# Kernel optimization log

Measured on AMD Instinct MI355X. Metric: run time of the kernel, lower is better.

## Reference

```python
import jax, jax.numpy as jnp
import numpy as np
import math

D_MODEL = 1024
N_HEADS = 16
D_K = D_MODEL // N_HEADS
BS, SQ, SK = 2, 2048, 2048


def setup_inputs() -> dict:
    key = jax.random.key(0)
    ks = jax.random.split(key, 7)
    q = jax.random.normal(ks[0], (BS, SQ, D_MODEL), dtype=jnp.float32)
    k = jax.random.normal(ks[1], (BS, SK, D_MODEL), dtype=jnp.float32)
    v = jax.random.normal(ks[2], (BS, SK, D_MODEL), dtype=jnp.float32)
    # causal mask: True = masked out (matches torch masked_fill semantics)
    mask = jnp.broadcast_to(
        ~jnp.tril(jnp.ones((SQ, SK), dtype=bool)), (BS, SQ, SK))
    scale = 1.0 / math.sqrt(D_MODEL)
    wq = jax.random.normal(ks[3], (D_MODEL, D_MODEL), dtype=jnp.float32) * scale
    wk = jax.random.normal(ks[4], (D_MODEL, D_MODEL), dtype=jnp.float32) * scale
    wv = jax.random.normal(ks[5], (D_MODEL, D_MODEL), dtype=jnp.float32) * scale
    wo = jax.random.normal(ks[6], (D_MODEL, D_MODEL), dtype=jnp.float32) * scale
    return {"q": q, "k": k, "v": v, "mask": mask,
            "wq": wq, "wk": wk, "wv": wv, "wo": wo}


def reference(q, k, v, mask, wq, wk, wv, wo):
    bs, sq, _ = q.shape
    sk = k.shape[1]
    # nn.Linear(bias=False): x @ W.T ; reshape to heads -> [b, h, s, d_k]
    qh = (q @ wq.T).reshape(bs, sq, N_HEADS, D_K).transpose(0, 2, 1, 3)
    kh = (k @ wk.T).reshape(bs, sk, N_HEADS, D_K).transpose(0, 2, 1, 3)
    vh = (v @ wv.T).reshape(bs, sk, N_HEADS, D_K).transpose(0, 2, 1, 3)
    # scaled dot-product attention, full [b,h,sq,sk] scores (as original)
    z = jnp.einsum('bhqd,bhkd->bhqk', qh, kh) / math.sqrt(D_K)
    z = jnp.where(mask[:, None, :, :], jnp.float32(-1e10), z)
    z = jax.nn.softmax(z, axis=-1)
    z = jnp.einsum('bhqk,bhkd->bhqd', z, vh)
    z = z.transpose(0, 2, 1, 3).reshape(bs, sq, D_MODEL)
    return z @ wo.T
```

## Files before the change

kernel.cpp:

```cpp
#include <hip/hip_runtime.h>
#include <hip/hip_bf16.h>
#include <stdint.h>

typedef short s16x8 __attribute__((ext_vector_type(8)));
typedef float f32x4 __attribute__((ext_vector_type(4)));

#define BSZ 2
#define SQL 2048
#define DMODEL 1024
#define NHEAD 16
#define DKH 64

#if __has_builtin(__builtin_amdgcn_exp2f)
#define EXP2(x) __builtin_amdgcn_exp2f(x)
#else
#define EXP2(x) exp2f(x)
#endif

__device__ __forceinline__ ushort f2bf(float f) {
  uint32_t u = __float_as_uint(f);
  u += 0x7fffu + ((u >> 16) & 1u);
  return (ushort)(u >> 16);
}

__device__ __forceinline__ uint32_t cvtpk_bf16(float lo, float hi) {
  uint32_t r;
  asm("v_cvt_pk_bf16_f32 %0, %1, %2" : "=v"(r) : "v"(lo), "v"(hi));
  return r;
}

__device__ __forceinline__ float rowmax16(float x) {
  x = fmaxf(x, __int_as_float(__builtin_amdgcn_update_dpp(0, __float_as_int(x), 0x121, 0xf, 0xf, true)));
  x = fmaxf(x, __int_as_float(__builtin_amdgcn_update_dpp(0, __float_as_int(x), 0x122, 0xf, 0xf, true)));
  x = fmaxf(x, __int_as_float(__builtin_amdgcn_update_dpp(0, __float_as_int(x), 0x124, 0xf, 0xf, true)));
  x = fmaxf(x, __int_as_float(__builtin_amdgcn_update_dpp(0, __float_as_int(x), 0x128, 0xf, 0xf, true)));
  return x;
}

__device__ __forceinline__ void gload_lds16(const ushort* g, ushort* l) {
  __builtin_amdgcn_global_load_lds((const __attribute__((address_space(1))) void*)g,
                                   (__attribute__((address_space(3))) void*)l,
                                   16, 0, 0);
}

__global__ void cvt_w(const float* __restrict__ wq, const float* __restrict__ wk,
                      const float* __restrict__ wv, const float* __restrict__ wo,
                      ushort* __restrict__ dwq, ushort* __restrict__ dwk,
                      ushort* __restrict__ dwv, ushort* __restrict__ dwo) {
  const float* s = (blockIdx.y == 0) ? wq : (blockIdx.y == 1) ? wk : (blockIdx.y == 2) ? wv : wo;
  ushort* d = (blockIdx.y == 0) ? dwq : (blockIdx.y == 1) ? dwk : (blockIdx.y == 2) ? dwv : dwo;
  int i = (blockIdx.x * 256 + threadIdx.x) * 4;
  float4 x = *(const float4*)(s + i);
  ushort4 o;
  o.x = f2bf(x.x); o.y = f2bf(x.y); o.z = f2bf(x.z); o.w = f2bf(x.w);
  *(ushort4*)(d + i) = o;
}

__device__ __forceinline__ void epi_heads(f32x4 (&acc)[4][4], ushort* D, float scale, bool vtrans) {
  const int lane = threadIdx.x & 63, w = threadIdx.x >> 6;
  const int m0 = blockIdx.x * 128, n0 = blockIdx.y * 128;
  const int wm = (w >> 1) * 64, wn = (w & 1) * 64;
#pragma unroll
  for (int mi = 0; mi < 4; ++mi)
#pragma unroll
    for (int ni = 0; ni < 4; ++ni)
#pragma unroll
      for (int r = 0; r < 4; ++r) {
        int m = m0 + wm + mi * 16 + (lane >> 4) * 4 + r;
        int n = n0 + wn + ni * 16 + (lane & 15);
        ushort bv = f2bf(acc[mi][ni][r] * scale);
        int b = m >> 11, s = m & 2047, h = n >> 6, d = n & 63;
        if (vtrans) {
          int sp = (s & ~63) | (((s & 15) << 2) | ((s >> 4) & 3));
          D[((size_t)((b * 16 + h) * 64 + d)) * 2048 + sp] = bv;
        } else {
          D[((size_t)((b * 16 + h) * 2048 + s)) * 64 + d] = bv;
        }
      }
}

__global__ __launch_bounds__(256) void gemm_qkv(const float* __restrict__ qf,
                                                const float* __restrict__ kf,
                                                const float* __restrict__ vf,
                                                const ushort* __restrict__ wqb,
                                                const ushort* __restrict__ wkb,
                                                const ushort* __restrict__ wvb,
                                                ushort* __restrict__ Qh,
                                                ushort* __restrict__ Kh,
                                                ushort* __restrict__ Vt) {
  __shared__ __align__(16) float sA32[2 * 4096];
  __shared__ __align__(16) ushort sB[2 * 4096];
  const int z = blockIdx.z;
  const float* A = (z == 0) ? qf : (z == 1) ? kf : vf;
  const ushort* B = (z == 0) ? wqb : (z == 1) ? wkb : wvb;
  const int t = threadIdx.x, w = t >> 6, lane = t & 63;
  const int lrow = lane & 15, g = lane >> 4;
  const int swzB = (lrow >> 1) & 3;
  const int m0 = blockIdx.x * 128, n0 = blockIdx.y * 128;
  const int wm = (w >> 1) * 64, wn = (w & 1) * 64;
  f32x4 acc[4][4] = {};

  auto stage = [&](int kt, int buf) {
#pragma unroll
    for (int i2 = 0; i2 < 4; ++i2) {
      int ci = i2 * 256 + t;
      int row = ci >> 3;
      int fc = (ci & 7) ^ (row & 7);
      gload_lds16((const ushort*)(A + (size_t)(m0 + row) * 1024 + kt * 32 + fc * 4),
                  (ushort*)(sA32 + buf * 4096 + (i2 * 256 + w * 64) * 4));
    }
#pragma unroll
    for (int i2 = 0; i2 < 2; ++i2) {
      int ci = i2 * 256 + t;
      int row = ci >> 2;
      int cs = (ci & 3) ^ ((row >> 1) & 3);
      gload_lds16(B + (size_t)(n0 + row) * 1024 + kt * 32 + cs * 8,
                  sB + buf * 4096 + (i2 * 256 + w * 64) * 8);
    }
  };

  stage(0, 0);
  for (int kt = 0; kt < 32; ++kt) {
    const int cur = kt & 1;
    if (kt < 31) {
      stage(kt + 1, cur ^ 1);
      asm volatile("s_waitcnt vmcnt(6)" ::: "memory");
    } else {
      asm volatile("s_waitcnt vmcnt(0)" ::: "memory");
    }
    __builtin_amdgcn_s_barrier();
    __builtin_amdgcn_sched_barrier(0);
    const float* pA = sA32 + cur * 4096;
    const ushort* pB = sB + cur * 4096;
    const int gs = (g ^ swzB) * 8;
    s16x8 af[4], bfr[4];
#pragma unroll
    for (int mi = 0; mi < 4; ++mi) {
      int row = wm + mi * 16 + lrow;
      int f0 = (2 * g) ^ (row & 7);
      int f1 = (2 * g + 1) ^ (row & 7);
      f32x4 x0 = *(const f32x4*)(pA + row * 32 + f0 * 4);
      f32x4 x1 = *(const f32x4*)(pA + row * 32 + f1 * 4);
      union { uint32_t u[4]; s16x8 v; } cc;
      cc.u[0] = cvtpk_bf16(x0[0], x0[1]);
      cc.u[1] = cvtpk_bf16(x0[2], x0[3]);
      cc.u[2] = cvtpk_bf16(x1[0], x1[1]);
      cc.u[3] = cvtpk_bf16(x1[2], x1[3]);
      af[mi] = cc.v;
    }
#pragma unroll
    for (int ni = 0; ni < 4; ++ni)
      bfr[ni] = *(const s16x8*)(pB + (wn + ni * 16 + lrow) * 32 + gs);
    __builtin_amdgcn_s_setprio(1);
#pragma unroll
    for (int mi = 0; mi < 4; ++mi)
#pragma unroll
      for (int ni = 0; ni < 4; ++ni)
        acc[mi][ni] = __builtin_amdgcn_mfma_f32_16x16x32_bf16(af[mi], bfr[ni], acc[mi][ni], 0, 0, 0);
    __builtin_amdgcn_s_setprio(0);
    asm volatile("s_waitcnt lgkmcnt(0)" ::: "memory");
    __builtin_amdgcn_s_barrier();
  }

  ushort* D = (z == 0) ? Qh : (z == 1) ? Kh : Vt;
  epi_heads(acc, D, (z == 0) ? 0.18033688f : 1.0f, z == 2);
}

__global__ __launch_bounds__(256) void gemm_out64(const ushort* __restrict__ A,
                                                  const ushort* __restrict__ B,
                                                  float* __restrict__ D) {
  __shared__ __align__(16) ushort sA[2 * 2048];
  __shared__ __align__(16) ushort sB[2 * 4096];
  const int t = threadIdx.x, w = t >> 6, lane = t & 63;
  const int lrow = lane & 15, g = lane >> 4;
  const int swz = (lrow >> 1) & 3;
  const int m0 = blockIdx.x * 64, n0 = blockIdx.y * 128;
  const int wm = (w >> 1) * 32, wn = (w & 1) * 64;
  f32x4 acc[2][4] = {};

  auto stage = [&](int kt, int buf) {
    {
      int row = t >> 2;
      int cs = (t & 3) ^ ((row >> 1) & 3);
      gload_lds16(A + (size_t)(m0 + row) * 1024 + kt * 32 + cs * 8,
                  sA + buf * 2048 + (w * 64) * 8);
    }
#pragma unroll
    for (int i2 = 0; i2 < 2; ++i2) {
      int ci = i2 * 256 + t;
      int row = ci >> 2;
      int cs = (ci & 3) ^ ((row >> 1) & 3);
      gload_lds16(B + (size_t)(n0 + row) * 1024 + kt * 32 + cs * 8,
                  sB + buf * 4096 + (i2 * 256 + w * 64) * 8);
    }
  };

  stage(0, 0);
  for (int kt = 0; kt < 32; ++kt) {
    const int cur = kt & 1;
    if (kt < 31) {
      stage(kt + 1, cur ^ 1);
      asm volatile("s_waitcnt vmcnt(3)" ::: "memory");
    } else {
      asm volatile("s_waitcnt vmcnt(0)" ::: "memory");
    }
    __builtin_amdgcn_s_barrier();
    __builtin_amdgcn_sched_barrier(0);
    const ushort* pA = sA + cur * 2048;
    const ushort* pB = sB + cur * 4096;
    const int gs = (g ^ swz) * 8;
    s16x8 af[2], bfr[4];
#pragma unroll
    for (int mi = 0; mi < 2; ++mi)
      af[mi] = *(const s16x8*)(pA + (wm + mi * 16 + lrow) * 32 + gs);
#pragma unroll
    for (int ni = 0; ni < 4; ++ni)
      bfr[ni] = *(const s16x8*)(pB + (wn + ni * 16 + lrow) * 32 + gs);
    __builtin_amdgcn_s_setprio(1);
#pragma unroll
    for (int mi = 0; mi < 2; ++mi)
#pragma unroll
      for (int ni = 0; ni < 4; ++ni)
        acc[mi][ni] = __builtin_amdgcn_mfma_f32_16x16x32_bf16(af[mi], bfr[ni], acc[mi][ni], 0, 0, 0);
    __builtin_amdgcn_s_setprio(0);
    asm volatile("s_waitcnt lgkmcnt(0)" ::: "memory");
    __builtin_amdgcn_s_barrier();
  }

#pragma unroll
  for (int mi = 0; mi < 2; ++mi)
#pragma unroll
    for (int ni = 0; ni < 4; ++ni)
#pragma unroll
      for (int r = 0; r < 4; ++r) {
        int m = m0 + wm + mi * 16 + (lane >> 4) * 4 + r;
        int n = n0 + wn + ni * 16 + (lane & 15);
        D[(size_t)m * 1024 + n] = acc[mi][ni][r];
      }
}

__global__ __launch_bounds__(512) void attn_fwd(const ushort* __restrict__ Qh,
                                                const ushort* __restrict__ Kh,
                                                const ushort* __restrict__ Vt,
                                                ushort* __restrict__ Z) {
  __shared__ __align__(16) ushort sK[2][64 * 64];
  __shared__ __align__(16) ushort sV[2][64 * 64];
  __shared__ __align__(16) ushort sP[8][16 * 72];
  const int t = threadIdx.x, w = t >> 6, lane = t & 63;
  const int lcol = lane & 15, lhi = lane >> 4;
  const int lid = blockIdx.x + 16 * blockIdx.y;
  const int p = lid >> 5;
  const int bh = (lid & 7) * 4 + ((lid >> 3) & 3);
  const int qlo = p, qhi = 31 - p;
  const int setid = w >> 2;
  const int qtile = setid ? qhi : qlo;
  const int qr0 = qtile * 64 + (w & 3) * 16;
  const ushort* Qb = Qh + (size_t)bh * SQL * DKH;
  const ushort* Kb = Kh + (size_t)bh * SQL * DKH;
  const ushort* Vb = Vt + (size_t)bh * DKH * SQL;

  s16x8 qf0, qf1;
  {
    const ushort* qp = Qb + (size_t)(qr0 + lcol) * DKH + lhi * 8;
    qf0 = *(const s16x8*)qp;
    qf1 = *(const s16x8*)(qp + 32);
  }
  float mr[4], lrp[4];
  f32x4 o[4] = {};
#pragma unroll
  for (int r = 0; r < 4; ++r) { mr[r] = -1e30f; lrp[r] = 0.f; }
  ushort* Pw = &sP[w][0];

  auto stage = [&](int kb, int buf) {
    int row = t >> 3, cc = t & 7;
    int scz = cc ^ (row & 7);
    gload_lds16(Kb + (size_t)(kb * 64 + row) * DKH + scz * 8, &sK[buf][w * 512]);
    gload_lds16(Vb + (size_t)row * SQL + kb * 64 + scz * 8, &sV[buf][w * 512]);
  };

  const int nkb = qhi + 1;
  stage(0, 0);
  for (int kb = 0; kb < nkb; ++kb) {
    const int cur = kb & 1;
    if (kb + 1 < nkb) {
      stage(kb + 1, cur ^ 1);
      asm volatile("s_waitcnt vmcnt(2)" ::: "memory");
    } else {
      asm volatile("s_waitcnt vmcnt(0)" ::: "memory");
    }
    __builtin_amdgcn_s_barrier();
    __builtin_amdgcn_sched_barrier(0);
    const bool act = setid || (kb <= qlo);
    if (act) {
      const ushort* pK = &sK[cur][0];
      const ushort* pV = &sV[cur][0];
      f32x4 sc4[4];
      __builtin_amdgcn_s_setprio(1);
#pragma unroll
      for (int ktt = 0; ktt < 4; ++ktt) {
        int row = ktt * 16 + lcol;
        int c0 = lhi ^ (row & 7);
        int c1 = (lhi + 4) ^ (row & 7);
        s16x8 k0 = *(const s16x8*)(pK + row * 64 + c0 * 8);
        s16x8 k1 = *(const s16x8*)(pK + row * 64 + c1 * 8);
        f32x4 a = {};
        a = __builtin_amdgcn_mfma_f32_16x16x32_bf16(qf0, k0, a, 0, 0, 0);
        a = __builtin_amdgcn_mfma_f32_16x16x32_bf16(qf1, k1, a, 0, 0, 0);
        sc4[ktt] = a;
      }
      __builtin_amdgcn_s_setprio(0);
      if (kb == qtile) {
#pragma unroll
        for (int ktt = 0; ktt < 4; ++ktt) {
          int kloc = ktt * 16 + lcol;
#pragma unroll
          for (int r = 0; r < 4; ++r)
            if (kloc > (w & 3) * 16 + lhi * 4 + r) sc4[ktt][r] = -1e30f;
        }
      }
      float tm4[4];
#pragma unroll
      for (int r = 0; r < 4; ++r) {
        float tm = fmaxf(fmaxf(sc4[0][r], sc4[1][r]), fmaxf(sc4[2][r], sc4[3][r]));
        tm4[r] = rowmax16(tm);
      }
      bool grow = (tm4[0] > mr[0] + 8.f) || (tm4[1] > mr[1] + 8.f) ||
                  (tm4[2] > mr[2] + 8.f) || (tm4[3] > mr[3] + 8.f);
      if (__any((int)grow)) {
#pragma unroll
        for (int r = 0; r < 4; ++r) {
          float mn = fmaxf(mr[r], tm4[r]);
          float al = EXP2(mr[r] - mn);
          lrp[r] *= al;
          o[0][r] *= al; o[1][r] *= al; o[2][r] *= al; o[3][r] *= al;
          mr[r] = mn;
        }
      }
#pragma unroll
      for (int r = 0; r < 4; ++r) {
        float p0 = EXP2(sc4[0][r] - mr[r]);
        float p1 = EXP2(sc4[1][r] - mr[r]);
        float p2 = EXP2(sc4[2][r] - mr[r]);
        float p3 = EXP2(sc4[3][r] - mr[r]);
        lrp[r] += (p0 + p1) + (p2 + p3);
        uint2 pk;
        pk.x = cvtpk_bf16(p0, p1);
        pk.y = cvtpk_bf16(p2, p3);
        *(uint2*)(Pw + (lhi * 4 + r) * 72 + lcol * 4) = pk;
      }
      __builtin_amdgcn_s_setprio(1);
#pragma unroll
      for (int kc = 0; kc < 2; ++kc) {
        s16x8 pf = *(const s16x8*)(Pw + lcol * 72 + kc * 32 + lhi * 8);
#pragma unroll
        for (int dt = 0; dt < 4; ++dt) {
          int row = dt * 16 + lcol;
          int cc = (lhi + 4 * kc) ^ (row & 7);
          s16x8 vf = *(const s16x8*)(pV + row * 64 + cc * 8);
          o[dt] = __builtin_amdgcn_mfma_f32_16x16x32_bf16(pf, vf, o[dt], 0, 0, 0);
        }
      }
      __builtin_amdgcn_s_setprio(0);
    }
    asm volatile("s_waitcnt lgkmcnt(0)" ::: "memory");
    __builtin_amdgcn_s_barrier();
  }

  const int b = bh >> 4, h = bh & 15;
#pragma unroll
  for (int r = 0; r < 4; ++r) {
    float sum = lrp[r];
    sum += __shfl_xor(sum, 1);
    sum += __shfl_xor(sum, 2);
    sum += __shfl_xor(sum, 4);
    sum += __shfl_xor(sum, 8);
    float inv = 1.0f / sum;
    int q = qr0 + lhi * 4 + r;
    size_t base = ((size_t)(b * SQL + q)) * DMODEL + h * DKH + lcol;
#pragma unroll
    for (int dt = 0; dt < 4; ++dt)
      Z[base + dt * 16] = f2bf(o[dt][r] * inv);
  }
}

extern "C" void kernel_launch(void* const* d_in, const int* in_sizes, int n_in,
                              void* d_out, int out_size, void* d_ws, size_t ws_size,
                              hipStream_t stream) {
  const float* q = (const float*)d_in[0];
  const float* k = (const float*)d_in[1];
  const float* v = (const float*)d_in[2];
  const float* wq = (const float*)d_in[4];
  const float* wk = (const float*)d_in[5];
  const float* wv = (const float*)d_in[6];
  const float* wo = (const float*)d_in[7];

  const size_t NBIG = (size_t)BSZ * SQL * DMODEL;
  const size_t NW = (size_t)DMODEL * DMODEL;
  ushort* wqb = (ushort*)d_ws;
  ushort* wkb = wqb + NW;
  ushort* wvb = wkb + NW;
  ushort* wob = wvb + NW;
  ushort* Qh = wob + NW;
  ushort* Kh = Qh + NBIG;
  ushort* Vt = Kh + NBIG;
  ushort* Z  = Vt + NBIG;

  cvt_w<<<dim3(1024, 4), 256, 0, stream>>>(wq, wk, wv, wo, wqb, wkb, wvb, wob);
  gemm_qkv<<<dim3(32, 8, 3), 256, 0, stream>>>(q, k, v, wqb, wkb, wvb, Qh, Kh, Vt);
  attn_fwd<<<dim3(16, BSZ * NHEAD), 512, 0, stream>>>(Qh, Kh, Vt, Z);
  gemm_out64<<<dim3(64, 8), 256, 0, stream>>>(Z, wob, (float*)d_out);
}
```

Baseline: 120.8 us.

## Convert QKV A-tiles to bf16 in registers before LDS store with prefetch

```diff
diff --git a/kernel.cpp b/kernel.cpp
--- a/kernel.cpp
+++ b/kernel.cpp
@@ -88,27 +88,44 @@
                                                 ushort* __restrict__ Qh,
                                                 ushort* __restrict__ Kh,
                                                 ushort* __restrict__ Vt) {
-  __shared__ __align__(16) float sA32[2 * 4096];
+  __shared__ __align__(16) ushort sA[2 * 4096];
   __shared__ __align__(16) ushort sB[2 * 4096];
   const int z = blockIdx.z;
   const float* A = (z == 0) ? qf : (z == 1) ? kf : vf;
   const ushort* B = (z == 0) ? wqb : (z == 1) ? wkb : wvb;
   const int t = threadIdx.x, w = t >> 6, lane = t & 63;
   const int lrow = lane & 15, g = lane >> 4;
-  const int swzB = (lrow >> 1) & 3;
+  const int swz = (lrow >> 1) & 3;
   const int m0 = blockIdx.x * 128, n0 = blockIdx.y * 128;
   const int wm = (w >> 1) * 64, wn = (w & 1) * 64;
   f32x4 acc[4][4] = {};
 
-  auto stage = [&](int kt, int buf) {
-#pragma unroll
-    for (int i2 = 0; i2 < 4; ++i2) {
-      int ci = i2 * 256 + t;
-      int row = ci >> 3;
-      int fc = (ci & 7) ^ (row & 7);
-      gload_lds16((const ushort*)(A + (size_t)(m0 + row) * 1024 + kt * 32 + fc * 4),
-                  (ushort*)(sA32 + buf * 4096 + (i2 * 256 + w * 64) * 4));
-    }
+  const int rA0 = t >> 2,         csA0 = (t & 3) ^ ((rA0 >> 1) & 3);
+  const int rA1 = (256 + t) >> 2, csA1 = (((256 + t) & 3)) ^ ((rA1 >> 1) & 3);
+  const float* Ap0 = A + (size_t)(m0 + rA0) * 1024 + csA0 * 8;
+  const float* Ap1 = A + (size_t)(m0 + rA1) * 1024 + csA1 * 8;
+
+  float4 ar[2][4];
+  auto issueA = [&](int kt, int slot) {
+    ar[slot][0] = *(const float4*)(Ap0 + kt * 32);
+    ar[slot][1] = *(const float4*)(Ap0 + kt * 32 + 4);
+    ar[slot][2] = *(const float4*)(Ap1 + kt * 32);
+    ar[slot][3] = *(const float4*)(Ap1 + kt * 32 + 4);
+  };
+  auto writeA = [&](int slot, int buf) {
+    uint4 u0, u1;
+    u0.x = cvtpk_bf16(ar[slot][0].x, ar[slot][0].y);
+    u0.y = cvtpk_bf16(ar[slot][0].z, ar[slot][0].w);
+    u0.z = cvtpk_bf16(ar[slot][1].x, ar[slot][1].y);
+    u0.w = cvtpk_bf16(ar[slot][1].z, ar[slot][1].w);
+    u1.x = cvtpk_bf16(ar[slot][2].x, ar[slot][2].y);
+    u1.y = cvtpk_bf16(ar[slot][2].z, ar[slot][2].w);
+    u1.z = cvtpk_bf16(ar[slot][3].x, ar[slot][3].y);
+    u1.w = cvtpk_bf16(ar[slot][3].z, ar[slot][3].w);
+    *(uint4*)(sA + buf * 4096 + t * 8) = u0;
+    *(uint4*)(sA + buf * 4096 + (256 + t) * 8) = u1;
+  };
+  auto gloadB = [&](int kt, int buf) {
 #pragma unroll
     for (int i2 = 0; i2 < 2; ++i2) {
       int ci = i2 * 256 + t;
@@ -119,35 +136,29 @@
     }
   };
 
-  stage(0, 0);
+  gloadB(0, 0);
+  issueA(0, 0);
+  issueA(1, 1);
+  writeA(0, 0);
+  asm volatile("s_waitcnt lgkmcnt(0)" ::: "memory");
+
   for (int kt = 0; kt < 32; ++kt) {
     const int cur = kt & 1;
     if (kt < 31) {
-      stage(kt + 1, cur ^ 1);
+      gloadB(kt + 1, cur ^ 1);
       asm volatile("s_waitcnt vmcnt(6)" ::: "memory");
     } else {
       asm volatile("s_waitcnt vmcnt(0)" ::: "memory");
     }
     __builtin_amdgcn_s_barrier();
     __builtin_amdgcn_sched_barrier(0);
-    const float* pA = sA32 + cur * 4096;
+    const ushort* pA = sA + cur * 4096;
     const ushort* pB = sB + cur * 4096;
-    const int gs = (g ^ swzB) * 8;
+    const int gs = (g ^ swz) * 8;
     s16x8 af[4], bfr[4];
 #pragma unroll
-    for (int mi = 0; mi < 4; ++mi) {
-      int row = wm + mi * 16 + lrow;
-      int f0 = (2 * g) ^ (row & 7);
-      int f1 = (2 * g + 1) ^ (row & 7);
-      f32x4 x0 = *(const f32x4*)(pA + row * 32 + f0 * 4);
-      f32x4 x1 = *(const f32x4*)(pA + row * 32 + f1 * 4);
-      union { uint32_t u[4]; s16x8 v; } cc;
-      cc.u[0] = cvtpk_bf16(x0[0], x0[1]);
-      cc.u[1] = cvtpk_bf16(x0[2], x0[3]);
-      cc.u[2] = cvtpk_bf16(x1[0], x1[1]);
-      cc.u[3] = cvtpk_bf16(x1[2], x1[3]);
-      af[mi] = cc.v;
-    }
+    for (int mi = 0; mi < 4; ++mi)
+      af[mi] = *(const s16x8*)(pA + (wm + mi * 16 + lrow) * 32 + gs);
 #pragma unroll
     for (int ni = 0; ni < 4; ++ni)
       bfr[ni] = *(const s16x8*)(pB + (wn + ni * 16 + lrow) * 32 + gs);
@@ -158,6 +169,8 @@
       for (int ni = 0; ni < 4; ++ni)
         acc[mi][ni] = __builtin_amdgcn_mfma_f32_16x16x32_bf16(af[mi], bfr[ni], acc[mi][ni], 0, 0, 0);
     __builtin_amdgcn_s_setprio(0);
+    if (kt < 31) writeA((kt + 1) & 1, cur ^ 1);
+    if (kt + 2 < 32) issueA(kt + 2, kt & 1);
     asm volatile("s_waitcnt lgkmcnt(0)" ::: "memory");
     __builtin_amdgcn_s_barrier();
   }
```

New measurement: 198.7 us. 1.64x slower.
